# Performance work log

Measured on AMD Instinct MI355X. Metric: run time of the kernel, lower is better.

## Reference

```python
import jax, jax.numpy as jnp
import numpy as np

NITER = 20  # clus_num_iters (faiss Kmeans niter)


def _kmeans_labels(X, init_idx, niter):
    """Lloyd's k-means on X [N,d] with centroids initialized at X[init_idx]; returns labels [N]."""
    def assign(cent):
        d2 = (cent * cent).sum(-1)[None, :] - 2.0 * (X @ cent.T)  # [N, C]
        return jnp.argmin(d2, axis=1)

    def step(cent, _):
        labels = assign(cent)
        C = cent.shape[0]
        sums = jax.ops.segment_sum(X, labels, num_segments=C)              # [C, d]
        counts = jax.ops.segment_sum(jnp.ones((X.shape[0],), X.dtype), labels, num_segments=C)
        new = jnp.where(counts[:, None] > 0, sums / jnp.maximum(counts, 1.0)[:, None], cent)
        return new, None

    cent0 = X[init_idx]
    cent, _ = jax.lax.scan(step, cent0, None, length=niter)
    return assign(cent)


def setup_inputs() -> dict:
    key = jax.random.key(0)
    k1, k2, k3, k4 = jax.random.split(key, 4)
    N, D, E, K, C = 8192, 256, 131072, 5, 64

    def l2norm(x):
        return x / jnp.linalg.norm(x, axis=-1, keepdims=True)

    # AFGRL passes F.normalize(student/teacher) into Neighbor
    student = l2norm(jax.random.normal(k1, (N, D), dtype=jnp.float32))
    teacher = l2norm(jax.random.normal(k2, (N, D), dtype=jnp.float32))
    edge_index = jax.random.randint(k3, (2, E), 0, N)          # sparse adj COO indices
    kmeans_init_idx = jax.random.randint(k4, (K, C), 0, N)     # per-seed centroid init
    return {
        "student": student,
        "teacher": teacher,
        "edge_index": edge_index,
        "kmeans_init_idx": kmeans_init_idx,
        "top_k": 8,
    }


def reference(student, teacher, edge_index, kmeans_init_idx, top_k):
    n = student.shape[0]
    idx = jnp.arange(n)

    # similarity with +10 on the diagonal (forces self as top-1 neighbor)
    sim = (student @ teacher.T).at[idx, idx].add(10.0)          # [n, n]
    D_knn, I_knn = jax.lax.top_k(sim, top_k)                    # [n, k], sorted desc

    # locality: knn edges that are also present in adj (sparse elementwise product)
    codes_adj = jnp.sort(edge_index[0] * n + edge_index[1])     # [E]
    codes_knn = (idx[:, None] * n + I_knn).ravel()              # [n*k]
    pos = jnp.clip(jnp.searchsorted(codes_adj, codes_knn), 0, codes_adj.shape[0] - 1)
    in_adj = (codes_adj[pos] == codes_knn).reshape(n, top_k)    # [n, k] bool

    # globality: knn edges whose endpoints share a cluster in ANY of the kmeans runs
    labels = jax.vmap(lambda ii: _kmeans_labels(teacher, ii, NITER))(kmeans_init_idx)  # [K, n]
    close = (labels[:, :, None] == labels[:, I_knn]).any(axis=0)  # [n, k] bool

    # pos_ = locality + globality ; coalesced indices == union of masked knn edges
    pos_mask = in_adj | close
    return I_knn, pos_mask, D_knn
```

## Files before the change

### kernel.cpp

```cpp
#include <hip/hip_runtime.h>
#include <hip/hip_bf16.h>
#include <math.h>

#define NN 8192
#define DD 256
#define KSEED 5
#define CC 64
#define TK 8
#define NITERS 20
#define CSPLIT 8
#define BM 128
#define BN 64
#define UB 32
#define NCAND 24
#define CPAD 257

typedef __attribute__((ext_vector_type(8))) short short8v;
typedef __attribute__((ext_vector_type(4))) float f32x4;

#define MFMA(a, b, c) __builtin_amdgcn_mfma_f32_16x16x32_bf16(a, b, c, 0, 0, 0)

__device__ __forceinline__ bool kbetter(float v1, int i1, float v2, int i2) {
    return (v1 > v2) || ((v1 == v2) && (i1 < i2));
}

__device__ __forceinline__ unsigned short f2bf(float x) {
    unsigned u = __float_as_uint(x);
    unsigned r = 0x7fffu + ((u >> 16) & 1u);
    return (unsigned short)((u + r) >> 16);
}
__device__ __forceinline__ float bf2f(unsigned short h) {
    return __uint_as_float(((unsigned)h) << 16);
}

__device__ __forceinline__ size_t fragidx(int row, int k) {
    return (((size_t)(row >> 4) * 8 + (k >> 5)) * 64 + ((k >> 3) & 3) * 16 + (row & 15)) * 8 + (k & 7);
}

__global__ __launch_bounds__(256) void adj_k(const int* __restrict__ e0,
                                             const int* __restrict__ e1,
                                             unsigned int* __restrict__ bm, int E) {
    int t = blockIdx.x * 256 + threadIdx.x;
    if (t < E) {
        unsigned code = (unsigned)e0[t] * NN + (unsigned)e1[t];
        atomicOr(&bm[code >> 5], 1u << (code & 31));
    }
}

__global__ __launch_bounds__(256) void conv_k(const float* __restrict__ src,
                                              short* __restrict__ hi,
                                              short* __restrict__ lo) {
    int slot = blockIdx.x * 256 + threadIdx.x;
    int l = slot & 63;
    int TS = slot >> 6;
    int S = TS & 7;
    int T = TS >> 3;
    int row = T * 16 + (l & 15);
    int k0 = S * 32 + (l >> 4) * 8;
    const float* p = src + (size_t)row * DD + k0;
    short8v h8, l8;
#pragma unroll
    for (int j = 0; j < 8; j++) {
        float x = p[j];
        unsigned short hb = f2bf(x);
        unsigned short lb = f2bf(x - bf2f(hb));
        h8[j] = (short)hb;
        l8[j] = (short)lb;
    }
    *(short8v*)(hi + (size_t)slot * 8) = h8;
    *(short8v*)(lo + (size_t)slot * 8) = l8;
}

__global__ __launch_bounds__(256) void kinit_k(const float* __restrict__ teacher,
                                               const int* __restrict__ initIdx,
                                               float* __restrict__ centR,
                                               float* __restrict__ cnorm,
                                               short* __restrict__ chi,
                                               short* __restrict__ clo) {
    int c = blockIdx.x, s = blockIdx.y;
    int t = threadIdx.x;
    int src = initIdx[s * CC + c];
    float v = teacher[(size_t)src * DD + t];
    centR[((size_t)s * CC + c) * DD + t] = v;
    unsigned short hb = f2bf(v);
    unsigned short lb = f2bf(v - bf2f(hb));
    size_t idx = (size_t)s * 16384 + fragidx(c, t);
    chi[idx] = (short)hb;
    clo[idx] = (short)lb;
    __shared__ float red[256];
    red[t] = v * v;
    __syncthreads();
    for (int w = 128; w > 0; w >>= 1) {
        if (t < w) red[t] += red[t + w];
        __syncthreads();
    }
    if (t == 0) cnorm[s * CC + c] = red[0];
}

__global__ __launch_bounds__(256) void kassign_k(const float* __restrict__ teacher,
                                                 const short* __restrict__ thi,
                                                 const short* __restrict__ tlo,
                                                 const short* __restrict__ chi,
                                                 const short* __restrict__ clo,
                                                 const float* __restrict__ centR,
                                                 const float* __restrict__ cnorm,
                                                 int* __restrict__ labels) {
    __shared__ float cent_s[CC * CPAD];
    __shared__ float cns[CC];
    const int s = blockIdx.y;
    const int pB = blockIdx.x * 64;
    const int tid = threadIdx.x;
    const int w = tid >> 6;
    const int lane = tid & 63;
    const int rl = lane & 15;
    const int lh = lane >> 4;
    {
        const float* src = centR + (size_t)s * CC * DD;
        for (int u = tid; u < CC * (DD / 4); u += 256) {
            int c = u >> 6;
            int q = (u & 63) << 2;
            float4 v = *(const float4*)&src[c * DD + q];
            float* dst = &cent_s[c * CPAD + q];
            dst[0] = v.x; dst[1] = v.y; dst[2] = v.z; dst[3] = v.w;
        }
    }
    if (tid < CC) cns[tid] = cnorm[s * CC + tid];
    __syncthreads();

    const short* chS = chi + (size_t)s * 16384;
    const short* clS = clo + (size_t)s * 16384;
    const int U = (pB >> 4) + w;

    f32x4 acc[4];
#pragma unroll
    for (int ct = 0; ct < 4; ct++) acc[ct] = (f32x4){0.f, 0.f, 0.f, 0.f};

#pragma unroll 1
    for (int S = 0; S < 8; S++) {
        const size_t boff = ((size_t)(U * 8 + S) * 64 + lane) * 8;
        short8v bh = *(const short8v*)(thi + boff);
        short8v bl = *(const short8v*)(tlo + boff);
#pragma unroll
        for (int ct = 0; ct < 4; ct++) {
            const size_t aoff = ((size_t)(ct * 8 + S) * 64 + lane) * 8;
            short8v ah = *(const short8v*)(chS + aoff);
            short8v al = *(const short8v*)(clS + aoff);
            acc[ct] = MFMA(ah, bh, acc[ct]);
            acc[ct] = MFMA(ah, bl, acc[ct]);
            acc[ct] = MFMA(al, bh, acc[ct]);
        }
    }

    float bd = INFINITY;
    int bc = 0;
#pragma unroll
    for (int ct = 0; ct < 4; ct++)
#pragma unroll
        for (int reg = 0; reg < 4; reg++) {
            int c = 16 * ct + 4 * lh + reg;
            float d = fmaf(-2.f, acc[ct][reg], cns[c]);
            if (d < bd) { bd = d; bc = c; }
        }
    const int gp = pB + 16 * w + rl;
    const float* tr = teacher + (size_t)gp * DD;
    const float* cr = &cent_s[bc * CPAD];
    float dot = 0.f;
    for (int k = 0; k < DD; k += 4) {
        float4 t4 = *(const float4*)&tr[k];
        dot = fmaf(t4.x, cr[k], dot);
        dot = fmaf(t4.y, cr[k + 1], dot);
        dot = fmaf(t4.z, cr[k + 2], dot);
        dot = fmaf(t4.w, cr[k + 3], dot);
    }
    float de = fmaf(-2.f, dot, cns[bc]);
#pragma unroll
    for (int off = 16; off <= 32; off <<= 1) {
        float od = __shfl_xor(de, off, 64);
        int oc = __shfl_xor(bc, off, 64);
        if (od < de || (od == de && oc < bc)) { de = od; bc = oc; }
    }
    if (lh == 0) labels[(size_t)s * NN + gp] = bc;
}

__global__ __launch_bounds__(256) void kupd12_k(const float* __restrict__ teacher,
                                                const int* __restrict__ labels,
                                                float* __restrict__ centR,
                                                float* __restrict__ cnorm,
                                                short* __restrict__ chi,
                                                short* __restrict__ clo) {
    const int c = blockIdx.x;
    const int s = blockIdx.y;
    const int t = threadIdx.x;
    __shared__ int list[NN];
    __shared__ float stage[UB * DD];
    __shared__ int scan_s[256];
    __shared__ float red[256];
    __shared__ int total_s;

    const int* labS = labels + (size_t)s * NN;

    int my = 0;
#pragma unroll
    for (int j = 0; j < 32; j++) my += (labS[t * 32 + j] == c);
    scan_s[t] = my;
    __syncthreads();
    for (int off = 1; off < 256; off <<= 1) {
        int v = (t >= off) ? scan_s[t - off] : 0;
        __syncthreads();
        scan_s[t] += v;
        __syncthreads();
    }
    const int base = scan_s[t] - my;
    if (t == 255) total_s = scan_s[255];
    int pos = base;
#pragma unroll
    for (int j = 0; j < 32; j++) {
        int p = t * 32 + j;
        if (labS[p] == c) list[pos++] = p;
    }
    __syncthreads();
    const int total = total_s;

    float sum = 0.f, part = 0.f;
    int curb = 0;
    for (int g0 = 0; g0 < total; g0 += UB) {
        const int gn = (total - g0 < UB) ? (total - g0) : UB;
        __syncthreads();
        for (int u = t; u < gn * (DD / 4); u += 256) {
            int j = u >> 6;
            int col4 = (u & 63) << 2;
            *(float4*)&stage[j * DD + col4] =
                *(const float4*)&teacher[(size_t)list[g0 + j] * DD + col4];
        }
        __syncthreads();
        for (int j = 0; j < gn; j++) {
            int p = list[g0 + j];
            int b = p >> 8;
            while (curb < b) { sum += part; part = 0.f; curb++; }
            part += stage[j * DD + t];
        }
    }
    while (curb < 32) { sum += part; part = 0.f; curb++; }

    float old = centR[((size_t)s * CC + c) * DD + t];
    float nv = (total > 0) ? (sum / (float)total) : old;
    centR[((size_t)s * CC + c) * DD + t] = nv;
    unsigned short hb = f2bf(nv);
    unsigned short lb = f2bf(nv - bf2f(hb));
    size_t idx = (size_t)s * 16384 + fragidx(c, t);
    chi[idx] = (short)hb;
    clo[idx] = (short)lb;
    red[t] = nv * nv;
    __syncthreads();
    for (int w = 128; w > 0; w >>= 1) {
        if (t < w) red[t] += red[t + w];
        __syncthreads();
    }
    if (t == 0) cnorm[s * CC + c] = red[0];
}

__global__ __launch_bounds__(256) void topk_gemm_k(const short* __restrict__ shi,
                                                   const short* __restrict__ slo,
                                                   const short* __restrict__ thi,
                                                   const short* __restrict__ tlo,
                                                   float* __restrict__ pv,
                                                   int* __restrict__ pi) {
    __shared__ float smem[BM * BN];

    const int split = blockIdx.x;
    const int rowB = blockIdx.y * BM;
    const int tid = threadIdx.x;
    const int w = tid >> 6;
    const int lane = tid & 63;
    const int rl = lane & 15;
    const int lh = lane >> 4;
    const int sr = tid >> 1;
    const int sh = tid & 1;

    float tv[TK];
    int ti[TK];
#pragma unroll
    for (int q = 0; q < TK; q++) { tv[q] = -INFINITY; ti[q] = 0x7fffffff; }

    const int colBase = split * (NN / CSPLIT);
    const int TA0 = (rowB >> 4) + 2 * w;

#pragma unroll 1
    for (int ct = 0; ct < (NN / CSPLIT) / BN; ct++) {
        const int colB = colBase + ct * BN;
        const int U0 = colB >> 4;
        f32x4 acc[2][4];
#pragma unroll
        for (int rt = 0; rt < 2; rt++)
#pragma unroll
            for (int ut = 0; ut < 4; ut++) acc[rt][ut] = (f32x4){0.f, 0.f, 0.f, 0.f};

#pragma unroll 1
        for (int S = 0; S < 8; S++) {
            const size_t a0off = ((size_t)(TA0 * 8 + S) * 64 + lane) * 8;
            const size_t a1off = ((size_t)((TA0 + 1) * 8 + S) * 64 + lane) * 8;
            short8v ah0 = *(const short8v*)(shi + a0off);
            short8v ah1 = *(const short8v*)(shi + a1off);
            short8v al0 = *(const short8v*)(slo + a0off);
            short8v al1 = *(const short8v*)(slo + a1off);
#pragma unroll
            for (int ut = 0; ut < 4; ut++) {
                const size_t boff = ((size_t)((U0 + ut) * 8 + S) * 64 + lane) * 8;
                short8v bh = *(const short8v*)(thi + boff);
                short8v bl = *(const short8v*)(tlo + boff);
                acc[0][ut] = MFMA(ah0, bh, acc[0][ut]);
                acc[0][ut] = MFMA(ah0, bl, acc[0][ut]);
                acc[0][ut] = MFMA(al0, bh, acc[0][ut]);
                acc[1][ut] = MFMA(ah1, bh, acc[1][ut]);
                acc[1][ut] = MFMA(ah1, bl, acc[1][ut]);
                acc[1][ut] = MFMA(al1, bh, acc[1][ut]);
            }
        }
        __syncthreads();
#pragma unroll
        for (int rt = 0; rt < 2; rt++)
#pragma unroll
            for (int ut = 0; ut < 4; ut++)
#pragma unroll
                for (int reg = 0; reg < 4; reg++) {
                    int r_loc = 32 * w + 16 * rt + 4 * lh + reg;
                    int cl = 16 * ut + rl;
                    float v = acc[rt][ut][reg];
                    if (rowB + r_loc == colB + cl) v += 10.f;
                    smem[r_loc * 64 + (cl ^ (r_loc & 31))] = v;
                }
        __syncthreads();
#pragma unroll 4
        for (int c = 0; c < 32; c++) {
            int cb2 = sh * 32 + c;
            float v = smem[sr * 64 + (cb2 ^ (sr & 31))];
            int gcol = colB + cb2;
            if (kbetter(v, gcol, tv[TK - 1], ti[TK - 1])) {
                tv[TK - 1] = v;
                ti[TK - 1] = gcol;
#pragma unroll
                for (int q = TK - 1; q > 0; --q) {
                    if (kbetter(tv[q], ti[q], tv[q - 1], ti[q - 1])) {
                        float t1 = tv[q]; tv[q] = tv[q - 1]; tv[q - 1] = t1;
                        int t2 = ti[q]; ti[q] = ti[q - 1]; ti[q - 1] = t2;
                    }
                }
            }
        }
    }
    int row = rowB + sr;
#pragma unroll
    for (int q = 0; q < TK; q++) {
        pv[((size_t)row * CSPLIT + split) * 16 + sh * 8 + q] = tv[q];
        pi[((size_t)row * CSPLIT + split) * 16 + sh * 8 + q] = ti[q];
    }
}

__global__ __launch_bounds__(256) void topk_merge_k(const float* __restrict__ pv,
                                                    const int* __restrict__ pi,
                                                    int* __restrict__ cand) {
    const int tid = threadIdx.x;
    const int wid = tid >> 6;
    const int lane = tid & 63;
    const int row = blockIdx.x * 4 + wid;
    const size_t base = (size_t)row * (CSPLIT * 16);

    float v0 = pv[base + lane];
    float v1 = pv[base + 64 + lane];
    unsigned i0 = (unsigned)pi[base + lane];
    unsigned i1 = (unsigned)pi[base + 64 + lane];
    unsigned s0 = __float_as_uint(v0);
    unsigned s1 = __float_as_uint(v1);
    unsigned m0 = (s0 & 0x80000000u) ? ~s0 : (s0 | 0x80000000u);
    unsigned m1 = (s1 & 0x80000000u) ? ~s1 : (s1 | 0x80000000u);
    unsigned long long k0 = (((unsigned long long)m0) << 32) | (0xFFFFFFFFu - i0);
    unsigned long long k1 = (((unsigned long long)m1) << 32) | (0xFFFFFFFFu - i1);

    for (int o = 0; o < NCAND; o++) {
        unsigned long long m = k0 > k1 ? k0 : k1;
#pragma unroll
        for (int off = 32; off > 0; off >>= 1) {
            unsigned long long other = __shfl_xor(m, off, 64);
            if (other > m) m = other;
        }
        if (lane == 0)
            cand[row * NCAND + o] = (int)(0xFFFFFFFFu - (unsigned)(m & 0xFFFFFFFFu));
        if (k0 == m) k0 = 0;
        if (k1 == m) k1 = 0;
    }
}

__global__ __launch_bounds__(256) void rescore_k(const float* __restrict__ student,
                                                 const float* __restrict__ teacher,
                                                 const int* __restrict__ cand,
                                                 int* __restrict__ iknn,
                                                 float* __restrict__ dknn) {
    __shared__ float srow[4 * DD];
    __shared__ int clist[4 * NCAND];
    __shared__ float cv[4 * NCAND];
    __shared__ int civ[4 * NCAND];
    const int tid = threadIdx.x;
    const int r0 = blockIdx.x * 4;
    *(float4*)&srow[tid * 4] = *(const float4*)&student[(size_t)r0 * DD + tid * 4];
    for (int i = tid; i < 4 * NCAND; i += 256) clist[i] = cand[r0 * NCAND + i];
    __syncthreads();
    const int w = tid >> 6;
    const int lane = tid & 63;
    const int r = r0 + w;
    if (lane < NCAND) {
        int c = clist[w * NCAND + lane];
        const float* tr = teacher + (size_t)c * DD;
        const float* sw = srow + w * DD;
        float acc = 0.f;
#pragma unroll 8
        for (int k = 0; k < DD; k += 4) {
            float4 t4 = *(const float4*)&tr[k];
            acc = fmaf(sw[k], t4.x, acc);
            acc = fmaf(sw[k + 1], t4.y, acc);
            acc = fmaf(sw[k + 2], t4.z, acc);
            acc = fmaf(sw[k + 3], t4.w, acc);
        }
        if (c == r) acc += 10.f;
        cv[w * NCAND + lane] = acc;
        civ[w * NCAND + lane] = c;
    }
    __syncthreads();
    if (lane == 0) {
        unsigned used = 0;
        for (int o = 0; o < TK; o++) {
            float bv = -INFINITY;
            int bi = 0x7fffffff;
            int bsel = -1;
            for (int m = 0; m < NCAND; m++) {
                if ((used >> m) & 1u) continue;
                float v = cv[w * NCAND + m];
                int ix = civ[w * NCAND + m];
                if (bsel < 0 || kbetter(v, ix, bv, bi)) { bv = v; bi = ix; bsel = m; }
            }
            used |= 1u << bsel;
            iknn[r * TK + o] = bi;
            dknn[r * TK + o] = bv;
        }
    }
}

__global__ __launch_bounds__(256) void out_k(const int* __restrict__ iknn,
                                             const float* __restrict__ dknn,
                                             const unsigned int* __restrict__ bm,
                                             const int* __restrict__ labels,
                                             float* __restrict__ out) {
    int t = blockIdx.x * 256 + threadIdx.x;
    int row = t >> 3;
    int ki = iknn[t];
    unsigned code = (unsigned)row * NN + (unsigned)ki;
    bool adj = (bm[code >> 5] >> (code & 31)) & 1u;
    bool close = false;
#pragma unroll
    for (int s = 0; s < KSEED; s++)
        close |= (labels[s * NN + row] == labels[s * NN + ki]);
    out[t] = (float)ki;
    out[NN * TK + t] = (adj || close) ? 1.0f : 0.0f;
    out[2 * NN * TK + t] = dknn[t];
}

extern "C" void kernel_launch(void* const* d_in, const int* in_sizes, int n_in,
                              void* d_out, int out_size, void* d_ws, size_t ws_size,
                              hipStream_t stream) {
    (void)n_in; (void)out_size; (void)ws_size;
    const float* student = (const float*)d_in[0];
    const float* teacher = (const float*)d_in[1];
    const int* edge = (const int*)d_in[2];
    const int* initIdx = (const int*)d_in[3];
    const int E = in_sizes[2] / 2;

    char* ws = (char*)d_ws;
    size_t off = 0;
    auto alloc = [&](size_t bytes) -> char* {
        char* p = ws + off;
        off += (bytes + 255) & ~(size_t)255;
        return p;
    };
    unsigned int* bm = (unsigned int*)alloc((size_t)NN * NN / 8);
    short* shi = (short*)alloc((size_t)NN * DD * 2);
    short* slo = (short*)alloc((size_t)NN * DD * 2);
    short* thi = (short*)alloc((size_t)NN * DD * 2);
    short* tlo = (short*)alloc((size_t)NN * DD * 2);
    float* centR = (float*)alloc((size_t)KSEED * CC * DD * 4);
    float* cnorm = (float*)alloc((size_t)KSEED * CC * 4);
    short* chi = (short*)alloc((size_t)KSEED * 16384 * 2);
    short* clo = (short*)alloc((size_t)KSEED * 16384 * 2);
    int* labels = (int*)alloc((size_t)KSEED * NN * 4);
    float* pv = (float*)alloc((size_t)NN * CSPLIT * 16 * 4);
    int* pi = (int*)alloc((size_t)NN * CSPLIT * 16 * 4);
    int* cand = (int*)alloc((size_t)NN * NCAND * 4);
    int* iknn = (int*)alloc((size_t)NN * TK * 4);
    float* dknn = (float*)alloc((size_t)NN * TK * 4);
    float* out = (float*)d_out;

    hipMemsetAsync(bm, 0, (size_t)NN * NN / 8, stream);
    adj_k<<<dim3((E + 255) / 256), 256, 0, stream>>>(edge, edge + E, bm, E);
    conv_k<<<dim3(NN * DD / 8 / 256), 256, 0, stream>>>(student, shi, slo);
    conv_k<<<dim3(NN * DD / 8 / 256), 256, 0, stream>>>(teacher, thi, tlo);

    kinit_k<<<dim3(CC, KSEED), 256, 0, stream>>>(teacher, initIdx, centR, cnorm, chi, clo);
    for (int it = 0; it < NITERS; ++it) {
        kassign_k<<<dim3(NN / 64, KSEED), 256, 0, stream>>>(teacher, thi, tlo, chi, clo,
                                                            centR, cnorm, labels);
        kupd12_k<<<dim3(CC, KSEED), 256, 0, stream>>>(teacher, labels, centR, cnorm, chi, clo);
    }
    kassign_k<<<dim3(NN / 64, KSEED), 256, 0, stream>>>(teacher, thi, tlo, chi, clo,
                                                        centR, cnorm, labels);

    topk_gemm_k<<<dim3(CSPLIT, NN / BM), 256, 0, stream>>>(shi, slo, thi, tlo, pv, pi);
    topk_merge_k<<<dim3(NN / 4), 256, 0, stream>>>(pv, pi, cand);
    rescore_k<<<dim3(NN / 4), 256, 0, stream>>>(student, teacher, cand, iknn, dknn);
    out_k<<<dim3(NN * TK / 256), 256, 0, stream>>>(iknn, dknn, bm, labels, out);
}
```

Measured before the change: 2.152 ms.

## Stage A row tile in LDS and halve row block to 64

Shrinks the top-k GEMM row block from 128 to 64 rows, so the grid doubles to 8x128 blocks and each wave now covers one 16-row tile instead of two. The block's whole A tile (hi and lo bf16 parts, 64 KB) is loaded once into shared memory, and the inner loop reads A fragments from there instead of global memory. Only half the threads now run the serial top-8 insertion scan. The aim is more parallelism and fewer repeated global A loads, but the extra LDS use (about 80 KB per block) limits occupancy, B traffic per output doubles, and half the threads sit idle during the scan.

Result: slower. 2.412 ms (+12.1%).

```diff
diff --git a/kernel.cpp b/kernel.cpp
--- a/kernel.cpp
+++ b/kernel.cpp
@@ -9,7 +9,7 @@
 #define TK 8
 #define NITERS 20
 #define CSPLIT 8
-#define BM 128
+#define BM 64
 #define BN 64
 #define UB 32
 #define NCAND 24
@@ -265,7 +265,9 @@
                                                    const short* __restrict__ tlo,
                                                    float* __restrict__ pv,
                                                    int* __restrict__ pi) {
-    __shared__ float smem[BM * BN];
+    __shared__ short Ah[16384];
+    __shared__ short Al[16384];
+    __shared__ float scanb[BM * BN];
 
     const int split = blockIdx.x;
     const int rowB = blockIdx.y * BM;
@@ -274,8 +276,17 @@
     const int lane = tid & 63;
     const int rl = lane & 15;
     const int lh = lane >> 4;
-    const int sr = tid >> 1;
-    const int sh = tid & 1;
+
+    {
+        const int TA0 = rowB >> 4;
+        const short* gH = shi + (size_t)TA0 * 4096;
+        const short* gL = slo + (size_t)TA0 * 4096;
+        for (int u = tid; u < 2048; u += 256) {
+            *(short8v*)&Ah[u * 8] = *(const short8v*)&gH[(size_t)u * 8];
+            *(short8v*)&Al[u * 8] = *(const short8v*)&gL[(size_t)u * 8];
+        }
+    }
+    __syncthreads();
 
     float tv[TK];
     int ti[TK];
@@ -283,76 +294,72 @@
     for (int q = 0; q < TK; q++) { tv[q] = -INFINITY; ti[q] = 0x7fffffff; }
 
     const int colBase = split * (NN / CSPLIT);
-    const int TA0 = (rowB >> 4) + 2 * w;
 
 #pragma unroll 1
     for (int ct = 0; ct < (NN / CSPLIT) / BN; ct++) {
         const int colB = colBase + ct * BN;
         const int U0 = colB >> 4;
-        f32x4 acc[2][4];
-#pragma unroll
-        for (int rt = 0; rt < 2; rt++)
-#pragma unroll
-            for (int ut = 0; ut < 4; ut++) acc[rt][ut] = (f32x4){0.f, 0.f, 0.f, 0.f};
+        f32x4 acc[4];
+#pragma unroll
+        for (int ut = 0; ut < 4; ut++) acc[ut] = (f32x4){0.f, 0.f, 0.f, 0.f};
 
 #pragma unroll 1
         for (int S = 0; S < 8; S++) {
-            const size_t a0off = ((size_t)(TA0 * 8 + S) * 64 + lane) * 8;
-            const size_t a1off = ((size_t)((TA0 + 1) * 8 + S) * 64 + lane) * 8;
-            short8v ah0 = *(const short8v*)(shi + a0off);
-            short8v ah1 = *(const short8v*)(shi + a1off);
-            short8v al0 = *(const short8v*)(slo + a0off);
-            short8v al1 = *(const short8v*)(slo + a1off);
+            short8v ah = *(const short8v*)&Ah[((w * 8 + S) * 64 + lane) * 8];
+            short8v al = *(const short8v*)&Al[((w * 8 + S) * 64 + lane) * 8];
 #pragma unroll
             for (int ut = 0; ut < 4; ut++) {
                 const size_t boff = ((size_t)((U0 + ut) * 8 + S) * 64 + lane) * 8;
                 short8v bh = *(const short8v*)(thi + boff);
                 short8v bl = *(const short8v*)(tlo + boff);
-                acc[0][ut] = MFMA(ah0, bh, acc[0][ut]);
-                acc[0][ut] = MFMA(ah0, bl, acc[0][ut]);
-                acc[0][ut] = MFMA(al0, bh, acc[0][ut]);
-                acc[1][ut] = MFMA(ah1, bh, acc[1][ut]);
-                acc[1][ut] = MFMA(ah1, bl, acc[1][ut]);
-                acc[1][ut] = MFMA(al1, bh, acc[1][ut]);
+                acc[ut] = MFMA(ah, bh, acc[ut]);
+                acc[ut] = MFMA(ah, bl, acc[ut]);
+                acc[ut] = MFMA(al, bh, acc[ut]);
             }
         }
         __syncthreads();
 #pragma unroll
-        for (int rt = 0; rt < 2; rt++)
-#pragma unroll
-            for (int ut = 0; ut < 4; ut++)
-#pragma unroll
-                for (int reg = 0; reg < 4; reg++) {
-                    int r_loc = 32 * w + 16 * rt + 4 * lh + reg;
-                    int cl = 16 * ut + rl;
-                    float v = acc[rt][ut][reg];
-                    if (rowB + r_loc == colB + cl) v += 10.f;
-                    smem[r_loc * 64 + (cl ^ (r_loc & 31))] = v;
-                }
-        __syncthreads();
+        for (int ut = 0; ut < 4; ut++)
+#pragma unroll
+            for (int reg = 0; reg < 4; reg++) {
+                int r_loc = 16 * w + 4 * lh + reg;
+                int cl = 16 * ut + rl;
+                float v = acc[ut][reg];
+                if (rowB + r_loc == colB + cl) v += 10.f;
+                scanb[r_loc * 64 + (cl ^ (r_loc & 31))] = v;
+            }
+        __syncthreads();
+        if (tid < 128) {
+            const int sr = tid >> 1;
+            const int sh = tid & 1;
 #pragma unroll 4
-        for (int c = 0; c < 32; c++) {
-            int cb2 = sh * 32 + c;
-            float v = smem[sr * 64 + (cb2 ^ (sr & 31))];
-            int gcol = colB + cb2;
-            if (kbetter(v, gcol, tv[TK - 1], ti[TK - 1])) {
-                tv[TK - 1] = v;
-                ti[TK - 1] = gcol;
-#pragma unroll
-                for (int q = TK - 1; q > 0; --q) {
-                    if (kbetter(tv[q], ti[q], tv[q - 1], ti[q - 1])) {
-                        float t1 = tv[q]; tv[q] = tv[q - 1]; tv[q - 1] = t1;
-                        int t2 = ti[q]; ti[q] = ti[q - 1]; ti[q - 1] = t2;
+            for (int c = 0; c < 32; c++) {
+                int cb2 = sh * 32 + c;
+                float v = scanb[sr * 64 + (cb2 ^ (sr & 31))];
+                int gcol = colB + cb2;
+                if (kbetter(v, gcol, tv[TK - 1], ti[TK - 1])) {
+                    tv[TK - 1] = v;
+                    ti[TK - 1] = gcol;
+#pragma unroll
+                    for (int q = TK - 1; q > 0; --q) {
+                        if (kbetter(tv[q], ti[q], tv[q - 1], ti[q - 1])) {
+                            float t1 = tv[q]; tv[q] = tv[q - 1]; tv[q - 1] = t1;
+                            int t2 = ti[q]; ti[q] = ti[q - 1]; ti[q - 1] = t2;
+                        }
                     }
                 }
             }
         }
     }
-    int row = rowB + sr;
-#pragma unroll
-    for (int q = 0; q < TK; q++) {
-        pv[((size_t)row * CSPLIT + split) * 16 + sh * 8 + q] = tv[q];
-        pi[((size_t)row * CSPLIT + split) * 16 + sh * 8 + q] = ti[q];
+    if (tid < 128) {
+        const int sr = tid >> 1;
+        const int sh = tid & 1;
+        int row = rowB + sr;
+#pragma unroll
+        for (int q = 0; q < TK; q++) {
+            pv[((size_t)row * CSPLIT + split) * 16 + sh * 8 + q] = tv[q];
+            pi[((size_t)row * CSPLIT + split) * 16 + sh * 8 + q] = ti[q];
+        }
     }
 }
 
```
